# Optimization experiments

Hardware: AMD Instinct MI355X
Metric: run time of the kernel (lower is better)

Reference implementation:

```python
import jax, jax.numpy as jnp
import numpy as np
import math

B, NQ, NK = 8, 1024, 2048
DQ = DK = DV = 1024
H = 8
DH = DV // H
EPS = 1e-5


def _layernorm(x, g, b):
    mu = jnp.mean(x, axis=-1, keepdims=True)
    var = jnp.mean(jnp.square(x - mu), axis=-1, keepdims=True)
    return (x - mu) * jax.lax.rsqrt(var + EPS) * g + b


def setup_inputs() -> dict:
    key = jax.random.key(0)
    ks = jax.random.split(key, 12)
    s_q = 1.0 / math.sqrt(DQ)
    s_v = 1.0 / math.sqrt(DV)
    return {
        "Q": jax.random.normal(ks[0], (B, NQ, DQ), jnp.float32),
        "K": jax.random.normal(ks[1], (B, NK, DK), jnp.float32),
        "Wq": jax.random.normal(ks[2], (DQ, DV), jnp.float32) * s_q,
        "bq": jnp.zeros((DV,), jnp.float32),
        "Wk": jax.random.normal(ks[3], (DK, DV), jnp.float32) * s_q,
        "bk": jnp.zeros((DV,), jnp.float32),
        "Wv": jax.random.normal(ks[4], (DK, DV), jnp.float32) * s_q,
        "bv": jnp.zeros((DV,), jnp.float32),
        "Wo": jax.random.normal(ks[5], (DV, DV), jnp.float32) * s_v,
        "bo": jnp.zeros((DV,), jnp.float32),
        "g0": jnp.ones((DV,), jnp.float32),
        "b0": jnp.zeros((DV,), jnp.float32),
        "g1": jnp.ones((DV,), jnp.float32),
        "b1": jnp.zeros((DV,), jnp.float32),
    }


def reference(Q, K, Wq, bq, Wk, bk, Wv, bv, Wo, bo, g0, b0, g1, b1):
    # projections
    q = Q @ Wq + bq                      # [B, NQ, DV]
    k = K @ Wk + bk                      # [B, NK, DV]
    v = K @ Wv + bv                      # [B, NK, DV]
    qh = q.reshape(B, NQ, H, DH)
    kh = k.reshape(B, NK, H, DH)
    vh = v.reshape(B, NK, H, DH)
    # NOTE: original scales by sqrt(dim_V), not sqrt(d_head)
    scale = 1.0 / math.sqrt(DV)
    logits = jnp.einsum("bqhd,bkhd->bhqk", qh, kh) * scale
    A = jax.nn.softmax(logits, axis=-1)
    # residual baked into attention output: Q_ + A @ V_
    Oh = qh + jnp.einsum("bhqk,bkhd->bqhd", A, vh)
    O = Oh.reshape(B, NQ, DV)
    O = _layernorm(O, g0, b0)
    O = O + jax.nn.relu(O @ Wo + bo)
    O = _layernorm(O, g1, b1)
    return O
```

## Files before the change

kernel.cpp:

```cpp
#include <hip/hip_runtime.h>
#include <stdint.h>

#define DEVI static __device__ __forceinline__

typedef __attribute__((ext_vector_type(8))) short short8;
typedef __attribute__((ext_vector_type(4))) float floatx4;
typedef __attribute__((ext_vector_type(4))) unsigned short ushortx4;

DEVI unsigned short f2bf(float f) {
  union { float f; uint32_t u; } v; v.f = f;
  uint32_t r = v.u + 0x7FFFu + ((v.u >> 16) & 1u);
  return (unsigned short)(r >> 16);
}
DEVI float bf2f(unsigned short s) {
  union { uint32_t u; float f; } v; v.u = ((uint32_t)s) << 16;
  return v.f;
}

DEVI void lds_cp16(void* lds, const void* g) {
  __builtin_amdgcn_global_load_lds(
      (const __attribute__((address_space(1))) uint32_t*)g,
      reinterpret_cast<__attribute__((address_space(3))) uint32_t*>(
          (uint32_t)reinterpret_cast<uintptr_t>(lds)),
      16, 0, 0);
}

__global__ __launch_bounds__(256) void cvt_qk(const float* __restrict__ Q,
                                              const float* __restrict__ K,
                                              unsigned short* __restrict__ Qb,
                                              unsigned short* __restrict__ Kb) {
  const int bid = blockIdx.x;
  const float* src;
  unsigned short* dst;
  size_t i;
  if (bid < 8192) { src = Q; dst = Qb; i = (size_t)bid * 256 + threadIdx.x; }
  else            { src = K; dst = Kb; i = (size_t)(bid - 8192) * 256 + threadIdx.x; }
  const floatx4 v = ((const floatx4*)src)[i];
  ushortx4 o;
  o.x = f2bf(v.x); o.y = f2bf(v.y); o.z = f2bf(v.z); o.w = f2bf(v.w);
  ((ushortx4*)dst)[i] = o;
}

__global__ __launch_bounds__(256) void wtrans4(const float* __restrict__ Wq,
                                               const float* __restrict__ Wk,
                                               const float* __restrict__ Wv,
                                               const float* __restrict__ Wo,
                                               unsigned short* __restrict__ Wt) {
  __shared__ float t[32][33];
  const int tx = threadIdx.x, ty = threadIdx.y;
  const int z = blockIdx.z;
  const float* W = (z == 0) ? Wq : (z == 1) ? Wk : (z == 2) ? Wv : Wo;
  unsigned short* D = Wt + (size_t)z * 1024 * 1024;
  const int c0 = blockIdx.x * 32, r0 = blockIdx.y * 32;
#pragma unroll
  for (int i = 0; i < 4; i++)
    t[ty + i * 8][tx] = W[(size_t)(r0 + ty + i * 8) * 1024 + c0 + tx];
  __syncthreads();
#pragma unroll
  for (int i = 0; i < 4; i++)
    D[(size_t)(c0 + ty + i * 8) * 1024 + r0 + tx] = f2bf(t[tx][ty + i * 8]);
}

template <int EPI>
__global__ __launch_bounds__(256, 3) void gemm_bt(
    const unsigned short* __restrict__ A, const unsigned short* __restrict__ Bt,
    const float* __restrict__ bias, const unsigned short* __restrict__ X1,
    void* __restrict__ Cout) {
  __shared__ unsigned short As[2][4][128][8];
  __shared__ unsigned short Bs[2][4][128][8];

  const int tid = threadIdx.x;
  const int lane = tid & 63, w = tid >> 6;
  const int wr = w >> 1, wc = w & 1;
  const int qd = lane >> 4, l16 = lane & 15;
  const int bid = blockIdx.x;
  const int xcd = bid & 7, loc = bid >> 3;
  const int m0 = (xcd * 8 + (loc & 7)) * 128;
  const int n0 = (loc >> 3) * 128;

  floatx4 acc[4][4];
#pragma unroll
  for (int i = 0; i < 4; i++)
#pragma unroll
    for (int j = 0; j < 4; j++) { floatx4 z = {0.f, 0.f, 0.f, 0.f}; acc[i][j] = z; }

  const int prow = tid & 127;
  const unsigned short* aptr = A + (size_t)(m0 + prow) * 1024 + ((tid >> 7) << 3);
  const unsigned short* bptr = Bt + (size_t)(n0 + prow) * 1024 + ((tid >> 7) << 3);
  const int dstoff = tid * 8;

  lds_cp16(&As[0][0][0][0] + dstoff, aptr);
  lds_cp16(&As[0][0][0][0] + dstoff + 2048, aptr + 16);
  lds_cp16(&Bs[0][0][0][0] + dstoff, bptr);
  lds_cp16(&Bs[0][0][0][0] + dstoff + 2048, bptr + 16);

  for (int it = 0; it < 32; it++) {
    __syncthreads();
    if (it < 31) {
      const int nb = (it + 1) & 1, k0 = (it + 1) * 32;
      lds_cp16(&As[nb][0][0][0] + dstoff, aptr + k0);
      lds_cp16(&As[nb][0][0][0] + dstoff + 2048, aptr + k0 + 16);
      lds_cp16(&Bs[nb][0][0][0] + dstoff, bptr + k0);
      lds_cp16(&Bs[nb][0][0][0] + dstoff + 2048, bptr + k0 + 16);
    }
    const int cur = it & 1;
    short8 af[4], bf[4];
#pragma unroll
    for (int mi = 0; mi < 4; mi++)
      af[mi] = *(const short8*)&As[cur][qd][wr * 64 + mi * 16 + l16][0];
#pragma unroll
    for (int ni = 0; ni < 4; ni++)
      bf[ni] = *(const short8*)&Bs[cur][qd][wc * 64 + ni * 16 + l16][0];
#pragma unroll
    for (int mi = 0; mi < 4; mi++)
#pragma unroll
      for (int ni = 0; ni < 4; ni++)
        acc[mi][ni] =
            __builtin_amdgcn_mfma_f32_16x16x32_bf16(af[mi], bf[ni], acc[mi][ni], 0, 0, 0);
  }

#pragma unroll
  for (int mi = 0; mi < 4; mi++) {
#pragma unroll
    for (int ni = 0; ni < 4; ni++) {
      const int row = m0 + wr * 64 + mi * 16 + qd * 4;
      const int col = n0 + wc * 64 + ni * 16 + l16;
      const float bv = bias[col];
      if constexpr (EPI == 0) {
        unsigned short* C = (unsigned short*)Cout;
#pragma unroll
        for (int r = 0; r < 4; r++)
          C[(size_t)(row + r) * 1024 + col] = f2bf(acc[mi][ni][r] + bv);
      } else {
        float* C = (float*)Cout;
#pragma unroll
        for (int r = 0; r < 4; r++) {
          const float x1 = bf2f(X1[(size_t)(row + r) * 1024 + col]);
          C[(size_t)(row + r) * 1024 + col] = x1 + fmaxf(acc[mi][ni][r] + bv, 0.f);
        }
      }
    }
  }
}

__global__ __launch_bounds__(512, 2) void gemm_kv(
    const unsigned short* __restrict__ A, const unsigned short* __restrict__ Bt,
    const float* __restrict__ biasK, const float* __restrict__ biasV,
    unsigned short* __restrict__ CK, unsigned short* __restrict__ CV) {
  __shared__ unsigned short As[2][4][256][8];
  __shared__ unsigned short Bs[2][4][256][8];

  const int tid = threadIdx.x;
  const int lane = tid & 63, w = tid >> 6;
  const int wr = w & 1, wc = w >> 1;
  const int qd = lane >> 4, l16 = lane & 15;
  const int bid = blockIdx.x;
  const int xcd = bid & 7, loc = bid >> 3;
  const int m0 = (xcd * 8 + (loc & 7)) * 256;
  const int n0 = (loc >> 3) * 256;

  floatx4 acc[8][4];
#pragma unroll
  for (int i = 0; i < 8; i++)
#pragma unroll
    for (int j = 0; j < 4; j++) { floatx4 z = {0.f, 0.f, 0.f, 0.f}; acc[i][j] = z; }

  const int r0 = tid & 255, c0 = tid >> 8;
  const unsigned short* aptr = A + (size_t)(m0 + r0) * 1024 + c0 * 8;
  const unsigned short* bptr = Bt + (size_t)(n0 + r0) * 1024 + c0 * 8;
  unsigned short* dstA = &As[0][c0][r0][0];
  unsigned short* dstB = &Bs[0][c0][r0][0];

  lds_cp16(dstA, aptr);
  lds_cp16(dstA + 4096, aptr + 16);
  lds_cp16(dstB, bptr);
  lds_cp16(dstB + 4096, bptr + 16);

  for (int it = 0; it < 32; it++) {
    __syncthreads();
    if (it < 31) {
      const int nb = (it + 1) & 1, k0 = (it + 1) * 32;
      lds_cp16(dstA + nb * 8192, aptr + k0);
      lds_cp16(dstA + nb * 8192 + 4096, aptr + k0 + 16);
      lds_cp16(dstB + nb * 8192, bptr + k0);
      lds_cp16(dstB + nb * 8192 + 4096, bptr + k0 + 16);
    }
    const int cur = it & 1;
    short8 af[8], bf[4];
#pragma unroll
    for (int mi = 0; mi < 8; mi++)
      af[mi] = *(const short8*)&As[cur][qd][wr * 128 + mi * 16 + l16][0];
#pragma unroll
    for (int ni = 0; ni < 4; ni++)
      bf[ni] = *(const short8*)&Bs[cur][qd][wc * 64 + ni * 16 + l16][0];
#pragma unroll
    for (int mi = 0; mi < 8; mi++)
#pragma unroll
      for (int ni = 0; ni < 4; ni++)
        acc[mi][ni] =
            __builtin_amdgcn_mfma_f32_16x16x32_bf16(af[mi], bf[ni], acc[mi][ni], 0, 0, 0);
  }

#pragma unroll
  for (int mi = 0; mi < 8; mi++) {
#pragma unroll
    for (int ni = 0; ni < 4; ni++) {
      const int row = m0 + wr * 128 + mi * 16 + qd * 4;
      const int col = n0 + wc * 64 + ni * 16 + l16;
      if (col < 1024) {
        const float bv = biasK[col];
#pragma unroll
        for (int r = 0; r < 4; r++)
          CK[(size_t)(row + r) * 1024 + col] = f2bf(acc[mi][ni][r] + bv);
      } else {
        const int vc = col - 1024;
        const float bv = biasV[vc];
        const int bb = row >> 11, nk = row & 2047;
        const int hh = vc >> 7, dh = vc & 127;
        ushortx4 pk;
        pk.x = f2bf(acc[mi][ni][0] + bv);
        pk.y = f2bf(acc[mi][ni][1] + bv);
        pk.z = f2bf(acc[mi][ni][2] + bv);
        pk.w = f2bf(acc[mi][ni][3] + bv);
        *(ushortx4*)&CV[(size_t)((bb * 8 + hh) * 128 + dh) * 2048 + nk] = pk;
      }
    }
  }
}

__global__ __launch_bounds__(256, 2) void attn(
    const unsigned short* __restrict__ qb, const unsigned short* __restrict__ kb,
    const unsigned short* __restrict__ vt, unsigned short* __restrict__ Ob) {
  __shared__ unsigned short smem[32768];

  const int tid = threadIdx.x;
  const int lane = tid & 63, w = tid >> 6;
  const int qd = lane >> 4, l16 = lane & 15;
  const int bid = blockIdx.x;
  const int qt = bid >> 6, bh = bid & 63;
  const int h = bh >> 3, b = bh & 7;
  const int m0 = qt * 128;

  const size_t qbase = ((size_t)(b * 1024 + m0)) * 1024 + h * 128;
  const size_t kbase = ((size_t)(b * 2048)) * 1024 + h * 128;
  const size_t vbase = ((size_t)((b * 8 + h) * 128)) * 2048;

#pragma unroll
  for (int i = 0; i < 8; i++) {
    const int p = i * 256 + tid;
    const int row = p & 127, c = p >> 7;
    lds_cp16(&smem[c * 1024 + row * 8], qb + qbase + (size_t)row * 1024 + c * 8);
  }
#pragma unroll
  for (int i = 0; i < 2; i++) {
    const int p = i * 256 + tid;
    const int kr = p & 31, kc = p >> 5;
    lds_cp16(&smem[16384 + kc * 256 + kr * 8], kb + kbase + (size_t)kr * 1024 + kc * 8);
    const int dh = p & 127, vc = p >> 7;
    lds_cp16(&smem[24576 + vc * 1024 + dh * 8], vt + vbase + (size_t)dh * 2048 + vc * 8);
  }
  __syncthreads();

  short8 qf[2][4];
#pragma unroll
  for (int mi = 0; mi < 2; mi++)
#pragma unroll
    for (int ks = 0; ks < 4; ks++)
      qf[mi][ks] =
          *(const short8*)&smem[(ks * 4 + qd) * 1024 + ((w * 2 + mi) * 16 + l16) * 8];
  __syncthreads();

  floatx4 oacc[2][8];
#pragma unroll
  for (int mi = 0; mi < 2; mi++)
#pragma unroll
    for (int ni = 0; ni < 8; ni++) { floatx4 z = {0.f, 0.f, 0.f, 0.f}; oacc[mi][ni] = z; }
  float lsum[2][4];
#pragma unroll
  for (int mi = 0; mi < 2; mi++)
#pragma unroll
    for (int r = 0; r < 4; r++) lsum[mi][r] = 0.f;

  for (int it = 0; it < 64; it++) {
    if (it) __syncthreads();
    if (it + 1 < 64) {
      const int nb = (it + 1) & 1, kv0 = (it + 1) * 32;
#pragma unroll
      for (int i = 0; i < 2; i++) {
        const int p = i * 256 + tid;
        const int kr = p & 31, kc = p >> 5;
        lds_cp16(&smem[16384 + nb * 4096 + kc * 256 + kr * 8],
                 kb + kbase + (size_t)(kv0 + kr) * 1024 + kc * 8);
        const int dh = p & 127, vc = p >> 7;
        lds_cp16(&smem[24576 + nb * 4096 + vc * 1024 + dh * 8],
                 vt + vbase + (size_t)dh * 2048 + kv0 + vc * 8);
      }
    }
    const int cur = it & 1;

    floatx4 sacc[2][2];
#pragma unroll
    for (int mi = 0; mi < 2; mi++)
#pragma unroll
      for (int ni = 0; ni < 2; ni++) { floatx4 z = {0.f, 0.f, 0.f, 0.f}; sacc[mi][ni] = z; }
#pragma unroll
    for (int ks = 0; ks < 4; ks++) {
      short8 b0 = *(const short8*)&smem[16384 + cur * 4096 + (ks * 4 + qd) * 256 + l16 * 8];
      short8 b1 =
          *(const short8*)&smem[16384 + cur * 4096 + (ks * 4 + qd) * 256 + (16 + l16) * 8];
#pragma unroll
      for (int mi = 0; mi < 2; mi++) {
        sacc[mi][0] = __builtin_amdgcn_mfma_f32_16x16x32_bf16(qf[mi][ks], b0, sacc[mi][0], 0, 0, 0);
        sacc[mi][1] = __builtin_amdgcn_mfma_f32_16x16x32_bf16(qf[mi][ks], b1, sacc[mi][1], 0, 0, 0);
      }
    }

#pragma unroll
    for (int mi = 0; mi < 2; mi++)
#pragma unroll
      for (int ni = 0; ni < 2; ni++) {
        const int kvl = ni * 16 + l16;
#pragma unroll
        for (int r = 0; r < 4; r++) {
          const float e = __expf(sacc[mi][ni][r] * 0.03125f);
          lsum[mi][r] += e;
          smem[(kvl >> 3) * 1024 + ((w * 2 + mi) * 16 + qd * 4 + r) * 8 + (kvl & 7)] = f2bf(e);
        }
      }

    short8 pf[2];
#pragma unroll
    for (int mi = 0; mi < 2; mi++)
      pf[mi] = *(const short8*)&smem[qd * 1024 + ((w * 2 + mi) * 16 + l16) * 8];
#pragma unroll
    for (int ni = 0; ni < 8; ni++) {
      const short8 vf = *(const short8*)&smem[24576 + cur * 4096 + qd * 1024 + (ni * 16 + l16) * 8];
#pragma unroll
      for (int mi = 0; mi < 2; mi++)
        oacc[mi][ni] = __builtin_amdgcn_mfma_f32_16x16x32_bf16(pf[mi], vf, oacc[mi][ni], 0, 0, 0);
    }
  }

  float inv[2][4];
#pragma unroll
  for (int mi = 0; mi < 2; mi++)
#pragma unroll
    for (int r = 0; r < 4; r++) {
      float s = lsum[mi][r];
      s += __shfl_xor(s, 1); s += __shfl_xor(s, 2);
      s += __shfl_xor(s, 4); s += __shfl_xor(s, 8);
      inv[mi][r] = 1.f / s;
    }

#pragma unroll
  for (int mi = 0; mi < 2; mi++)
#pragma unroll
    for (int ni = 0; ni < 8; ni++)
#pragma unroll
      for (int r = 0; r < 4; r++) {
        const int m = (w * 2 + mi) * 16 + qd * 4 + r;
        const int dh = ni * 16 + l16;
        const float qv = bf2f(qb[qbase + (size_t)m * 1024 + dh]);
        Ob[qbase + (size_t)m * 1024 + dh] = f2bf(qv + oacc[mi][ni][r] * inv[mi][r]);
      }
}

__global__ __launch_bounds__(256) void ln_rows(const unsigned short* __restrict__ X,
                                               const float* __restrict__ g,
                                               const float* __restrict__ bb,
                                               unsigned short* __restrict__ Y) {
  __shared__ float red[8];
  const int row = blockIdx.x, tid = threadIdx.x;
  const int w = tid >> 6, lane = tid & 63;
  const ushortx4 u = ((const ushortx4*)(X + (size_t)row * 1024))[tid];
  float x0 = bf2f(u.x), x1 = bf2f(u.y), x2 = bf2f(u.z), x3 = bf2f(u.w);
  float s = x0 + x1 + x2 + x3;
  float s2 = x0 * x0 + x1 * x1 + x2 * x2 + x3 * x3;
#pragma unroll
  for (int off = 1; off < 64; off <<= 1) { s += __shfl_xor(s, off); s2 += __shfl_xor(s2, off); }
  if (lane == 0) { red[w] = s; red[4 + w] = s2; }
  __syncthreads();
  s = red[0] + red[1] + red[2] + red[3];
  s2 = red[4] + red[5] + red[6] + red[7];
  const float mu = s * (1.f / 1024.f);
  const float rs = rsqrtf(s2 * (1.f / 1024.f) - mu * mu + 1e-5f);
  const floatx4 gv = ((const floatx4*)g)[tid];
  const floatx4 bv = ((const floatx4*)bb)[tid];
  ushortx4 o;
  o.x = f2bf((x0 - mu) * rs * gv.x + bv.x);
  o.y = f2bf((x1 - mu) * rs * gv.y + bv.y);
  o.z = f2bf((x2 - mu) * rs * gv.z + bv.z);
  o.w = f2bf((x3 - mu) * rs * gv.w + bv.w);
  ((ushortx4*)(Y + (size_t)row * 1024))[tid] = o;
}

__global__ __launch_bounds__(256) void ln_f32(const float* __restrict__ X,
                                              const float* __restrict__ g,
                                              const float* __restrict__ bb,
                                              float* __restrict__ out) {
  __shared__ float red[8];
  const int row = blockIdx.x, tid = threadIdx.x;
  const int w = tid >> 6, lane = tid & 63;
  const floatx4 xv = ((const floatx4*)(X + (size_t)row * 1024))[tid];
  float x0 = xv.x, x1 = xv.y, x2 = xv.z, x3 = xv.w;
  float s = x0 + x1 + x2 + x3;
  float s2 = x0 * x0 + x1 * x1 + x2 * x2 + x3 * x3;
#pragma unroll
  for (int off = 1; off < 64; off <<= 1) { s += __shfl_xor(s, off); s2 += __shfl_xor(s2, off); }
  if (lane == 0) { red[w] = s; red[4 + w] = s2; }
  __syncthreads();
  s = red[0] + red[1] + red[2] + red[3];
  s2 = red[4] + red[5] + red[6] + red[7];
  const float mu = s * (1.f / 1024.f);
  const float rs = rsqrtf(s2 * (1.f / 1024.f) - mu * mu + 1e-5f);
  const floatx4 gv = ((const floatx4*)g)[tid];
  const floatx4 bv = ((const floatx4*)bb)[tid];
  floatx4 o;
  o.x = (x0 - mu) * rs * gv.x + bv.x;
  o.y = (x1 - mu) * rs * gv.y + bv.y;
  o.z = (x2 - mu) * rs * gv.z + bv.z;
  o.w = (x3 - mu) * rs * gv.w + bv.w;
  ((floatx4*)(out + (size_t)row * 1024))[tid] = o;
}

extern "C" void kernel_launch(void* const* d_in, const int* in_sizes, int n_in,
                              void* d_out, int out_size, void* d_ws, size_t ws_size,
                              hipStream_t stream) {
  (void)in_sizes; (void)n_in; (void)out_size; (void)ws_size;
  const float* Q  = (const float*)d_in[0];
  const float* K  = (const float*)d_in[1];
  const float* Wq = (const float*)d_in[2];
  const float* bq = (const float*)d_in[3];
  const float* Wk = (const float*)d_in[4];
  const float* bk = (const float*)d_in[5];
  const float* Wv = (const float*)d_in[6];
  const float* bv = (const float*)d_in[7];
  const float* Wo = (const float*)d_in[8];
  const float* bo = (const float*)d_in[9];
  const float* g0 = (const float*)d_in[10];
  const float* b0 = (const float*)d_in[11];
  const float* g1 = (const float*)d_in[12];
  const float* b1 = (const float*)d_in[13];
  float* out = (float*)d_out;

  char* ws = (char*)d_ws;
  const size_t MB = 1u << 20;
  unsigned short* Qb  = (unsigned short*)(ws + 0);
  unsigned short* Kb  = (unsigned short*)(ws + 16 * MB);
  unsigned short* Wt  = (unsigned short*)(ws + 48 * MB);
  unsigned short* qbp = (unsigned short*)(ws + 56 * MB);
  unsigned short* kbp = (unsigned short*)(ws + 72 * MB);
  unsigned short* vtp = (unsigned short*)(ws + 104 * MB);
  unsigned short* O   = Qb;
  unsigned short* X1  = Kb;
  float* O2 = (float*)(ws + 72 * MB);

  unsigned short* Wqt  = Wt;
  unsigned short* Wkvt = Wt + (size_t)1024 * 1024;
  unsigned short* Wot  = Wt + (size_t)3072 * 1024;

  cvt_qk<<<24576, 256, 0, stream>>>(Q, K, Qb, Kb);
  wtrans4<<<dim3(32, 32, 4), dim3(32, 8), 0, stream>>>(Wq, Wk, Wv, Wo, Wt);

  gemm_bt<0><<<512, 256, 0, stream>>>(Qb, Wqt, bq, nullptr, qbp);
  gemm_kv<<<512, 512, 0, stream>>>(Kb, Wkvt, bk, bv, kbp, vtp);
  attn<<<512, 256, 0, stream>>>(qbp, kbp, vtp, O);
  ln_rows<<<8192, 256, 0, stream>>>(O, g0, b0, X1);
  gemm_bt<2><<<512, 256, 0, stream>>>(X1, Wot, bo, X1, O2);
  ln_f32<<<8192, 256, 0, stream>>>(O2, g1, b1, out);
}
```

Before: 478.7 us.

## Replace LDS-staged GEMM and attention loads with direct global register loads

Removes the LDS double-buffering (global_load_lds plus syncthreads) from the Q/O projection GEMMs, the KV projection GEMM and the attention kernel. Each wave now loads its MFMA fragments straight from global memory into registers, with a two-stage register ping-pong in the GEMMs. The KV GEMM also moves from 256x256 tiles with 512 threads to 128x128 tiles with 256 threads. This drops barrier and LDS traffic, but loses the cross-wave data sharing that LDS gave, so global and L2 traffic and uncoalesced 16-byte row loads increase.

New measurement: 800.5 us. 1.67x slower.

```diff
diff --git a/kernel.cpp b/kernel.cpp
--- a/kernel.cpp
+++ b/kernel.cpp
@@ -15,14 +15,6 @@
 DEVI float bf2f(unsigned short s) {
   union { uint32_t u; float f; } v; v.u = ((uint32_t)s) << 16;
   return v.f;
-}
-
-DEVI void lds_cp16(void* lds, const void* g) {
-  __builtin_amdgcn_global_load_lds(
-      (const __attribute__((address_space(1))) uint32_t*)g,
-      reinterpret_cast<__attribute__((address_space(3))) uint32_t*>(
-          (uint32_t)reinterpret_cast<uintptr_t>(lds)),
-      16, 0, 0);
 }
 
 __global__ __launch_bounds__(256) void cvt_qk(const float* __restrict__ Q,
@@ -61,22 +53,38 @@
     D[(size_t)(c0 + ty + i * 8) * 1024 + r0 + tx] = f2bf(t[tx][ty + i * 8]);
 }
 
-template <int EPI>
-__global__ __launch_bounds__(256, 3) void gemm_bt(
+#define LD_AB(av, bv, K0)                                                      \
+  {                                                                            \
+    _Pragma("unroll") for (int i = 0; i < 4; i++) {                            \
+      av[i] = *(const short8*)(ap + (size_t)i * 16384 + (K0));                 \
+      bv[i] = *(const short8*)(bp + (size_t)i * 16384 + (K0));                 \
+    }                                                                          \
+  }
+#define MFMA16(av, bv)                                                         \
+  {                                                                            \
+    _Pragma("unroll") for (int mi = 0; mi < 4; mi++)                           \
+        _Pragma("unroll") for (int ni = 0; ni < 4; ni++) acc[mi][ni] =         \
+        __builtin_amdgcn_mfma_f32_16x16x32_bf16(av[mi], bv[ni], acc[mi][ni],   \
+                                                0, 0, 0);                      \
+  }
+
+template <int EPI, int BSH>
+__global__ __launch_bounds__(256, 2) void gemm_rd(
     const unsigned short* __restrict__ A, const unsigned short* __restrict__ Bt,
     const float* __restrict__ bias, const unsigned short* __restrict__ X1,
     void* __restrict__ Cout) {
-  __shared__ unsigned short As[2][4][128][8];
-  __shared__ unsigned short Bs[2][4][128][8];
-
   const int tid = threadIdx.x;
   const int lane = tid & 63, w = tid >> 6;
   const int wr = w >> 1, wc = w & 1;
   const int qd = lane >> 4, l16 = lane & 15;
   const int bid = blockIdx.x;
   const int xcd = bid & 7, loc = bid >> 3;
-  const int m0 = (xcd * 8 + (loc & 7)) * 128;
-  const int n0 = (loc >> 3) * 128;
+  const int mt = xcd * (1 << BSH) + (loc & ((1 << BSH) - 1));
+  const int nt = loc >> BSH;
+  const int m0 = mt * 128, n0 = nt * 128;
+
+  const unsigned short* ap = A + (size_t)(m0 + wr * 64 + l16) * 1024 + qd * 8;
+  const unsigned short* bp = Bt + (size_t)(n0 + wc * 64 + l16) * 1024 + qd * 8;
 
   floatx4 acc[4][4];
 #pragma unroll
@@ -84,39 +92,13 @@
 #pragma unroll
     for (int j = 0; j < 4; j++) { floatx4 z = {0.f, 0.f, 0.f, 0.f}; acc[i][j] = z; }
 
-  const int prow = tid & 127;
-  const unsigned short* aptr = A + (size_t)(m0 + prow) * 1024 + ((tid >> 7) << 3);
-  const unsigned short* bptr = Bt + (size_t)(n0 + prow) * 1024 + ((tid >> 7) << 3);
-  const int dstoff = tid * 8;
-
-  lds_cp16(&As[0][0][0][0] + dstoff, aptr);
-  lds_cp16(&As[0][0][0][0] + dstoff + 2048, aptr + 16);
-  lds_cp16(&Bs[0][0][0][0] + dstoff, bptr);
-  lds_cp16(&Bs[0][0][0][0] + dstoff + 2048, bptr + 16);
-
-  for (int it = 0; it < 32; it++) {
-    __syncthreads();
-    if (it < 31) {
-      const int nb = (it + 1) & 1, k0 = (it + 1) * 32;
-      lds_cp16(&As[nb][0][0][0] + dstoff, aptr + k0);
-      lds_cp16(&As[nb][0][0][0] + dstoff + 2048, aptr + k0 + 16);
-      lds_cp16(&Bs[nb][0][0][0] + dstoff, bptr + k0);
-      lds_cp16(&Bs[nb][0][0][0] + dstoff + 2048, bptr + k0 + 16);
-    }
-    const int cur = it & 1;
-    short8 af[4], bf[4];
-#pragma unroll
-    for (int mi = 0; mi < 4; mi++)
-      af[mi] = *(const short8*)&As[cur][qd][wr * 64 + mi * 16 + l16][0];
-#pragma unroll
-    for (int ni = 0; ni < 4; ni++)
-      bf[ni] = *(const short8*)&Bs[cur][qd][wc * 64 + ni * 16 + l16][0];
-#pragma unroll
-    for (int mi = 0; mi < 4; mi++)
-#pragma unroll
-      for (int ni = 0; ni < 4; ni++)
-        acc[mi][ni] =
-            __builtin_amdgcn_mfma_f32_16x16x32_bf16(af[mi], bf[ni], acc[mi][ni], 0, 0, 0);
+  short8 a0[4], b0[4], a1[4], b1[4];
+  LD_AB(a0, b0, 0)
+  for (int it = 0; it < 32; it += 2) {
+    LD_AB(a1, b1, (it + 1) * 32)
+    MFMA16(a0, b0)
+    if (it + 2 < 32) LD_AB(a0, b0, (it + 2) * 32)
+    MFMA16(a1, b1)
   }
 
 #pragma unroll
@@ -143,69 +125,43 @@
   }
 }
 
-__global__ __launch_bounds__(512, 2) void gemm_kv(
+__global__ __launch_bounds__(256, 2) void gemm_kv_rd(
     const unsigned short* __restrict__ A, const unsigned short* __restrict__ Bt,
     const float* __restrict__ biasK, const float* __restrict__ biasV,
     unsigned short* __restrict__ CK, unsigned short* __restrict__ CV) {
-  __shared__ unsigned short As[2][4][256][8];
-  __shared__ unsigned short Bs[2][4][256][8];
-
   const int tid = threadIdx.x;
   const int lane = tid & 63, w = tid >> 6;
-  const int wr = w & 1, wc = w >> 1;
+  const int wr = w >> 1, wc = w & 1;
   const int qd = lane >> 4, l16 = lane & 15;
   const int bid = blockIdx.x;
   const int xcd = bid & 7, loc = bid >> 3;
-  const int m0 = (xcd * 8 + (loc & 7)) * 256;
-  const int n0 = (loc >> 3) * 256;
-
-  floatx4 acc[8][4];
-#pragma unroll
-  for (int i = 0; i < 8; i++)
+  const int mt = xcd * 16 + (loc & 15);
+  const int nt = loc >> 4;
+  const int m0 = mt * 128, n0 = nt * 128;
+
+  const unsigned short* ap = A + (size_t)(m0 + wr * 64 + l16) * 1024 + qd * 8;
+  const unsigned short* bp = Bt + (size_t)(n0 + wc * 64 + l16) * 1024 + qd * 8;
+
+  floatx4 acc[4][4];
+#pragma unroll
+  for (int i = 0; i < 4; i++)
 #pragma unroll
     for (int j = 0; j < 4; j++) { floatx4 z = {0.f, 0.f, 0.f, 0.f}; acc[i][j] = z; }
 
-  const int r0 = tid & 255, c0 = tid >> 8;
-  const unsigned short* aptr = A + (size_t)(m0 + r0) * 1024 + c0 * 8;
-  const unsigned short* bptr = Bt + (size_t)(n0 + r0) * 1024 + c0 * 8;
-  unsigned short* dstA = &As[0][c0][r0][0];
-  unsigned short* dstB = &Bs[0][c0][r0][0];
-
-  lds_cp16(dstA, aptr);
-  lds_cp16(dstA + 4096, aptr + 16);
-  lds_cp16(dstB, bptr);
-  lds_cp16(dstB + 4096, bptr + 16);
-
-  for (int it = 0; it < 32; it++) {
-    __syncthreads();
-    if (it < 31) {
-      const int nb = (it + 1) & 1, k0 = (it + 1) * 32;
-      lds_cp16(dstA + nb * 8192, aptr + k0);
-      lds_cp16(dstA + nb * 8192 + 4096, aptr + k0 + 16);
-      lds_cp16(dstB + nb * 8192, bptr + k0);
-      lds_cp16(dstB + nb * 8192 + 4096, bptr + k0 + 16);
-    }
-    const int cur = it & 1;
-    short8 af[8], bf[4];
-#pragma unroll
-    for (int mi = 0; mi < 8; mi++)
-      af[mi] = *(const short8*)&As[cur][qd][wr * 128 + mi * 16 + l16][0];
-#pragma unroll
-    for (int ni = 0; ni < 4; ni++)
-      bf[ni] = *(const short8*)&Bs[cur][qd][wc * 64 + ni * 16 + l16][0];
-#pragma unroll
-    for (int mi = 0; mi < 8; mi++)
-#pragma unroll
-      for (int ni = 0; ni < 4; ni++)
-        acc[mi][ni] =
-            __builtin_amdgcn_mfma_f32_16x16x32_bf16(af[mi], bf[ni], acc[mi][ni], 0, 0, 0);
-  }
-
-#pragma unroll
-  for (int mi = 0; mi < 8; mi++) {
+  short8 a0[4], b0[4], a1[4], b1[4];
+  LD_AB(a0, b0, 0)
+  for (int it = 0; it < 32; it += 2) {
+    LD_AB(a1, b1, (it + 1) * 32)
+    MFMA16(a0, b0)
+    if (it + 2 < 32) LD_AB(a0, b0, (it + 2) * 32)
+    MFMA16(a1, b1)
+  }
+
+#pragma unroll
+  for (int mi = 0; mi < 4; mi++) {
 #pragma unroll
     for (int ni = 0; ni < 4; ni++) {
-      const int row = m0 + wr * 128 + mi * 16 + qd * 4;
+      const int row = m0 + wr * 64 + mi * 16 + qd * 4;
       const int col = n0 + wc * 64 + ni * 16 + l16;
       if (col < 1024) {
         const float bv = biasK[col];
@@ -231,7 +187,7 @@
 __global__ __launch_bounds__(256, 2) void attn(
     const unsigned short* __restrict__ qb, const unsigned short* __restrict__ kb,
     const unsigned short* __restrict__ vt, unsigned short* __restrict__ Ob) {
-  __shared__ unsigned short smem[32768];
+  __shared__ unsigned short Ps[4096];
 
   const int tid = threadIdx.x;
   const int lane = tid & 63, w = tid >> 6;
@@ -245,30 +201,16 @@
   const size_t kbase = ((size_t)(b * 2048)) * 1024 + h * 128;
   const size_t vbase = ((size_t)((b * 8 + h) * 128)) * 2048;
 
-#pragma unroll
-  for (int i = 0; i < 8; i++) {
-    const int p = i * 256 + tid;
-    const int row = p & 127, c = p >> 7;
-    lds_cp16(&smem[c * 1024 + row * 8], qb + qbase + (size_t)row * 1024 + c * 8);
-  }
-#pragma unroll
-  for (int i = 0; i < 2; i++) {
-    const int p = i * 256 + tid;
-    const int kr = p & 31, kc = p >> 5;
-    lds_cp16(&smem[16384 + kc * 256 + kr * 8], kb + kbase + (size_t)kr * 1024 + kc * 8);
-    const int dh = p & 127, vc = p >> 7;
-    lds_cp16(&smem[24576 + vc * 1024 + dh * 8], vt + vbase + (size_t)dh * 2048 + vc * 8);
-  }
-  __syncthreads();
-
+  const unsigned short* qp = qb + qbase + (size_t)(w * 32 + l16) * 1024 + qd * 8;
   short8 qf[2][4];
 #pragma unroll
   for (int mi = 0; mi < 2; mi++)
 #pragma unroll
     for (int ks = 0; ks < 4; ks++)
-      qf[mi][ks] =
-          *(const short8*)&smem[(ks * 4 + qd) * 1024 + ((w * 2 + mi) * 16 + l16) * 8];
-  __syncthreads();
+      qf[mi][ks] = *(const short8*)(qp + (size_t)mi * 16384 + ks * 32);
+
+  const unsigned short* kp = kb + kbase + (size_t)l16 * 1024 + qd * 8;
+  const unsigned short* vp = vt + vbase + (size_t)l16 * 2048 + qd * 8;
 
   floatx4 oacc[2][8];
 #pragma unroll
@@ -282,21 +224,7 @@
     for (int r = 0; r < 4; r++) lsum[mi][r] = 0.f;
 
   for (int it = 0; it < 64; it++) {
-    if (it) __syncthreads();
-    if (it + 1 < 64) {
-      const int nb = (it + 1) & 1, kv0 = (it + 1) * 32;
-#pragma unroll
-      for (int i = 0; i < 2; i++) {
-        const int p = i * 256 + tid;
-        const int kr = p & 31, kc = p >> 5;
-        lds_cp16(&smem[16384 + nb * 4096 + kc * 256 + kr * 8],
-                 kb + kbase + (size_t)(kv0 + kr) * 1024 + kc * 8);
-        const int dh = p & 127, vc = p >> 7;
-        lds_cp16(&smem[24576 + nb * 4096 + vc * 1024 + dh * 8],
-                 vt + vbase + (size_t)dh * 2048 + kv0 + vc * 8);
-      }
-    }
-    const int cur = it & 1;
+    const int kv0 = it * 32;
 
     floatx4 sacc[2][2];
 #pragma unroll
@@ -305,13 +233,12 @@
       for (int ni = 0; ni < 2; ni++) { floatx4 z = {0.f, 0.f, 0.f, 0.f}; sacc[mi][ni] = z; }
 #pragma unroll
     for (int ks = 0; ks < 4; ks++) {
-      short8 b0 = *(const short8*)&smem[16384 + cur * 4096 + (ks * 4 + qd) * 256 + l16 * 8];
-      short8 b1 =
-          *(const short8*)&smem[16384 + cur * 4096 + (ks * 4 + qd) * 256 + (16 + l16) * 8];
+      const short8 k0f = *(const short8*)(kp + (size_t)kv0 * 1024 + ks * 32);
+      const short8 k1f = *(const short8*)(kp + (size_t)(kv0 + 16) * 1024 + ks * 32);
 #pragma unroll
       for (int mi = 0; mi < 2; mi++) {
-        sacc[mi][0] = __builtin_amdgcn_mfma_f32_16x16x32_bf16(qf[mi][ks], b0, sacc[mi][0], 0, 0, 0);
-        sacc[mi][1] = __builtin_amdgcn_mfma_f32_16x16x32_bf16(qf[mi][ks], b1, sacc[mi][1], 0, 0, 0);
+        sacc[mi][0] = __builtin_amdgcn_mfma_f32_16x16x32_bf16(qf[mi][ks], k0f, sacc[mi][0], 0, 0, 0);
+        sacc[mi][1] = __builtin_amdgcn_mfma_f32_16x16x32_bf16(qf[mi][ks], k1f, sacc[mi][1], 0, 0, 0);
       }
     }
 
@@ -324,17 +251,17 @@
         for (int r = 0; r < 4; r++) {
           const float e = __expf(sacc[mi][ni][r] * 0.03125f);
           lsum[mi][r] += e;
-          smem[(kvl >> 3) * 1024 + ((w * 2 + mi) * 16 + qd * 4 + r) * 8 + (kvl & 7)] = f2bf(e);
+          Ps[(kvl >> 3) * 1024 + (w * 32 + mi * 16 + qd * 4 + r) * 8 + (kvl & 7)] = f2bf(e);
         }
       }
 
     short8 pf[2];
 #pragma unroll
     for (int mi = 0; mi < 2; mi++)
-      pf[mi] = *(const short8*)&smem[qd * 1024 + ((w * 2 + mi) * 16 + l16) * 8];
+      pf[mi] = *(const short8*)&Ps[qd * 1024 + (w * 32 + mi * 16 + l16) * 8];
 #pragma unroll
     for (int ni = 0; ni < 8; ni++) {
-      const short8 vf = *(const short8*)&smem[24576 + cur * 4096 + qd * 1024 + (ni * 16 + l16) * 8];
+      const short8 vf = *(const short8*)(vp + (size_t)ni * 32768 + kv0);
 #pragma unroll
       for (int mi = 0; mi < 2; mi++)
         oacc[mi][ni] = __builtin_amdgcn_mfma_f32_16x16x32_bf16(pf[mi], vf, oacc[mi][ni], 0, 0, 0);
@@ -358,7 +285,7 @@
     for (int ni = 0; ni < 8; ni++)
 #pragma unroll
       for (int r = 0; r < 4; r++) {
-        const int m = (w * 2 + mi) * 16 + qd * 4 + r;
+        const int m = w * 32 + mi * 16 + qd * 4 + r;
         const int dh = ni * 16 + l16;
         const float qv = bf2f(qb[qbase + (size_t)m * 1024 + dh]);
         Ob[qbase + (size_t)m * 1024 + dh] = f2bf(qv + oacc[mi][ni][r] * inv[mi][r]);
@@ -462,10 +389,10 @@
   cvt_qk<<<24576, 256, 0, stream>>>(Q, K, Qb, Kb);
   wtrans4<<<dim3(32, 32, 4), dim3(32, 8), 0, stream>>>(Wq, Wk, Wv, Wo, Wt);
 
-  gemm_bt<0><<<512, 256, 0, stream>>>(Qb, Wqt, bq, nullptr, qbp);
-  gemm_kv<<<512, 512, 0, stream>>>(Kb, Wkvt, bk, bv, kbp, vtp);
+  gemm_rd<0, 3><<<512, 256, 0, stream>>>(Qb, Wqt, bq, nullptr, qbp);
+  gemm_kv_rd<<<2048, 256, 0, stream>>>(Kb, Wkvt, bk, bv, kbp, vtp);
   attn<<<512, 256, 0, stream>>>(qbp, kbp, vtp, O);
   ln_rows<<<8192, 256, 0, stream>>>(O, g0, b0, X1);
-  gemm_bt<2><<<512, 256, 0, stream>>>(X1, Wot, bo, X1, O2);
+  gemm_rd<2, 3><<<512, 256, 0, stream>>>(X1, Wot, bo, X1, O2);
   ln_f32<<<8192, 256, 0, stream>>>(O2, g1, b1, out);
 }
```

## Run K/V projection GEMM in FP8 with smaller tiles

Applied to the files above, without the earlier changes.

Converts K and the Wk/Wv weights to FP8 instead of bf16 and replaces the bf16 K/V projection GEMM with an FP8 MFMA kernel using 128x128 tiles, 256 threads and 2048 blocks. This halves the bytes for the K input and weights and doubles MFMA throughput per instruction. The workspace layout is rearranged accordingly. It risks accuracy loss from FP8 quantisation of K and the weights, which feed both the attention logits and the values.

New measurement: 437.9 us. -8.5%, faster.

```diff
diff --git a/kernel.cpp b/kernel.cpp
--- a/kernel.cpp
+++ b/kernel.cpp
@@ -15,6 +15,9 @@
 DEVI float bf2f(unsigned short s) {
   union { uint32_t u; float f; } v; v.u = ((uint32_t)s) << 16;
   return v.f;
+}
+DEVI unsigned char f2fp8(float f) {
+  return (unsigned char)(__builtin_amdgcn_cvt_pk_fp8_f32(f, f, 0, false) & 0xff);
 }
 
 DEVI void lds_cp16(void* lds, const void* g) {
@@ -28,37 +31,49 @@
 __global__ __launch_bounds__(256) void cvt_qk(const float* __restrict__ Q,
                                               const float* __restrict__ K,
                                               unsigned short* __restrict__ Qb,
-                                              unsigned short* __restrict__ Kb) {
+                                              unsigned char* __restrict__ Kf8) {
   const int bid = blockIdx.x;
-  const float* src;
-  unsigned short* dst;
-  size_t i;
-  if (bid < 8192) { src = Q; dst = Qb; i = (size_t)bid * 256 + threadIdx.x; }
-  else            { src = K; dst = Kb; i = (size_t)(bid - 8192) * 256 + threadIdx.x; }
-  const floatx4 v = ((const floatx4*)src)[i];
-  ushortx4 o;
-  o.x = f2bf(v.x); o.y = f2bf(v.y); o.z = f2bf(v.z); o.w = f2bf(v.w);
-  ((ushortx4*)dst)[i] = o;
+  if (bid < 8192) {
+    const size_t i = (size_t)bid * 256 + threadIdx.x;
+    const floatx4 v = ((const floatx4*)Q)[i];
+    ushortx4 o;
+    o.x = f2bf(v.x); o.y = f2bf(v.y); o.z = f2bf(v.z); o.w = f2bf(v.w);
+    ((ushortx4*)Qb)[i] = o;
+  } else {
+    const size_t i = (size_t)(bid - 8192) * 256 + threadIdx.x;
+    const floatx4 v = ((const floatx4*)K)[i];
+    int p = __builtin_amdgcn_cvt_pk_fp8_f32(v.x, v.y, 0, false);
+    p = __builtin_amdgcn_cvt_pk_fp8_f32(v.z, v.w, p, true);
+    ((int*)Kf8)[i] = p;
+  }
 }
 
 __global__ __launch_bounds__(256) void wtrans4(const float* __restrict__ Wq,
                                                const float* __restrict__ Wk,
                                                const float* __restrict__ Wv,
                                                const float* __restrict__ Wo,
-                                               unsigned short* __restrict__ Wt) {
+                                               unsigned short* __restrict__ Wt,
+                                               unsigned char* __restrict__ Wt8) {
   __shared__ float t[32][33];
   const int tx = threadIdx.x, ty = threadIdx.y;
   const int z = blockIdx.z;
   const float* W = (z == 0) ? Wq : (z == 1) ? Wk : (z == 2) ? Wv : Wo;
-  unsigned short* D = Wt + (size_t)z * 1024 * 1024;
   const int c0 = blockIdx.x * 32, r0 = blockIdx.y * 32;
 #pragma unroll
   for (int i = 0; i < 4; i++)
     t[ty + i * 8][tx] = W[(size_t)(r0 + ty + i * 8) * 1024 + c0 + tx];
   __syncthreads();
-#pragma unroll
-  for (int i = 0; i < 4; i++)
-    D[(size_t)(c0 + ty + i * 8) * 1024 + r0 + tx] = f2bf(t[tx][ty + i * 8]);
+  if (z == 0 || z == 3) {
+    unsigned short* D = Wt + (z == 0 ? 0 : (size_t)1024 * 1024);
+#pragma unroll
+    for (int i = 0; i < 4; i++)
+      D[(size_t)(c0 + ty + i * 8) * 1024 + r0 + tx] = f2bf(t[tx][ty + i * 8]);
+  } else {
+    unsigned char* D = Wt8 + (z == 1 ? 0 : (size_t)1024 * 1024);
+#pragma unroll
+    for (int i = 0; i < 4; i++)
+      D[(size_t)(c0 + ty + i * 8) * 1024 + r0 + tx] = f2fp8(t[tx][ty + i * 8]);
+  }
 }
 
 template <int EPI>
@@ -143,69 +158,82 @@
   }
 }
 
-__global__ __launch_bounds__(512, 2) void gemm_kv(
-    const unsigned short* __restrict__ A, const unsigned short* __restrict__ Bt,
+__global__ __launch_bounds__(256, 3) void gemm_kv_f8(
+    const unsigned char* __restrict__ A, const unsigned char* __restrict__ Bt,
     const float* __restrict__ biasK, const float* __restrict__ biasV,
     unsigned short* __restrict__ CK, unsigned short* __restrict__ CV) {
-  __shared__ unsigned short As[2][4][256][8];
-  __shared__ unsigned short Bs[2][4][256][8];
+  __shared__ unsigned char As[2][4][128][16];
+  __shared__ unsigned char Bs[2][4][128][16];
 
   const int tid = threadIdx.x;
   const int lane = tid & 63, w = tid >> 6;
-  const int wr = w & 1, wc = w >> 1;
+  const int wr = w >> 1, wc = w & 1;
   const int qd = lane >> 4, l16 = lane & 15;
   const int bid = blockIdx.x;
   const int xcd = bid & 7, loc = bid >> 3;
-  const int m0 = (xcd * 8 + (loc & 7)) * 256;
-  const int n0 = (loc >> 3) * 256;
-
-  floatx4 acc[8][4];
-#pragma unroll
-  for (int i = 0; i < 8; i++)
+  const int m0 = (xcd * 16 + (loc & 15)) * 128;
+  const int n0 = (loc >> 4) * 128;
+
+  floatx4 acc[4][4];
+#pragma unroll
+  for (int i = 0; i < 4; i++)
 #pragma unroll
     for (int j = 0; j < 4; j++) { floatx4 z = {0.f, 0.f, 0.f, 0.f}; acc[i][j] = z; }
 
-  const int r0 = tid & 255, c0 = tid >> 8;
-  const unsigned short* aptr = A + (size_t)(m0 + r0) * 1024 + c0 * 8;
-  const unsigned short* bptr = Bt + (size_t)(n0 + r0) * 1024 + c0 * 8;
-  unsigned short* dstA = &As[0][c0][r0][0];
-  unsigned short* dstB = &Bs[0][c0][r0][0];
-
-  lds_cp16(dstA, aptr);
-  lds_cp16(dstA + 4096, aptr + 16);
-  lds_cp16(dstB, bptr);
-  lds_cp16(dstB + 4096, bptr + 16);
-
-  for (int it = 0; it < 32; it++) {
+  const int srow = tid & 127, sc = tid >> 7;
+  const unsigned char* aptr = A + (size_t)(m0 + srow) * 1024 + sc * 16;
+  const unsigned char* bptr = Bt + (size_t)(n0 + srow) * 1024 + sc * 16;
+  unsigned char* dA = &As[0][sc][srow][0];
+  unsigned char* dB = &Bs[0][sc][srow][0];
+
+  lds_cp16(dA, aptr);
+  lds_cp16(dA + 4096, aptr + 32);
+  lds_cp16(dB, bptr);
+  lds_cp16(dB + 4096, bptr + 32);
+
+  for (int it = 0; it < 16; it++) {
     __syncthreads();
-    if (it < 31) {
-      const int nb = (it + 1) & 1, k0 = (it + 1) * 32;
-      lds_cp16(dstA + nb * 8192, aptr + k0);
-      lds_cp16(dstA + nb * 8192 + 4096, aptr + k0 + 16);
-      lds_cp16(dstB + nb * 8192, bptr + k0);
-      lds_cp16(dstB + nb * 8192 + 4096, bptr + k0 + 16);
+    if (it < 15) {
+      const int nb = (it + 1) & 1, k0 = (it + 1) * 64;
+      lds_cp16(dA + nb * 8192, aptr + k0);
+      lds_cp16(dA + nb * 8192 + 4096, aptr + k0 + 32);
+      lds_cp16(dB + nb * 8192, bptr + k0);
+      lds_cp16(dB + nb * 8192 + 4096, bptr + k0 + 32);
     }
     const int cur = it & 1;
-    short8 af[8], bf[4];
-#pragma unroll
-    for (int mi = 0; mi < 8; mi++)
-      af[mi] = *(const short8*)&As[cur][qd][wr * 128 + mi * 16 + l16][0];
-#pragma unroll
-    for (int ni = 0; ni < 4; ni++)
-      bf[ni] = *(const short8*)&Bs[cur][qd][wc * 64 + ni * 16 + l16][0];
-#pragma unroll
-    for (int mi = 0; mi < 8; mi++)
+    const int coff = (qd & 1) * 8, chi = qd >> 1;
+    long a8[4][2], b8[4][2];
+#pragma unroll
+    for (int mi = 0; mi < 4; mi++) {
+      const int row = wr * 64 + mi * 16 + l16;
+      a8[mi][0] = *(const long*)&As[cur][chi][row][coff];
+      a8[mi][1] = *(const long*)&As[cur][2 + chi][row][coff];
+    }
+#pragma unroll
+    for (int ni = 0; ni < 4; ni++) {
+      const int row = wc * 64 + ni * 16 + l16;
+      b8[ni][0] = *(const long*)&Bs[cur][chi][row][coff];
+      b8[ni][1] = *(const long*)&Bs[cur][2 + chi][row][coff];
+    }
+#pragma unroll
+    for (int mi = 0; mi < 4; mi++)
 #pragma unroll
       for (int ni = 0; ni < 4; ni++)
-        acc[mi][ni] =
-            __builtin_amdgcn_mfma_f32_16x16x32_bf16(af[mi], bf[ni], acc[mi][ni], 0, 0, 0);
-  }
-
-#pragma unroll
-  for (int mi = 0; mi < 8; mi++) {
+        acc[mi][ni] = __builtin_amdgcn_mfma_f32_16x16x32_fp8_fp8(
+            a8[mi][0], b8[ni][0], acc[mi][ni], 0, 0, 0);
+#pragma unroll
+    for (int mi = 0; mi < 4; mi++)
+#pragma unroll
+      for (int ni = 0; ni < 4; ni++)
+        acc[mi][ni] = __builtin_amdgcn_mfma_f32_16x16x32_fp8_fp8(
+            a8[mi][1], b8[ni][1], acc[mi][ni], 0, 0, 0);
+  }
+
+#pragma unroll
+  for (int mi = 0; mi < 4; mi++) {
 #pragma unroll
     for (int ni = 0; ni < 4; ni++) {
-      const int row = m0 + wr * 128 + mi * 16 + qd * 4;
+      const int row = m0 + wr * 64 + mi * 16 + qd * 4;
       const int col = n0 + wc * 64 + ni * 16 + l16;
       if (col < 1024) {
         const float bv = biasK[col];
@@ -446,24 +474,24 @@
   char* ws = (char*)d_ws;
   const size_t MB = 1u << 20;
   unsigned short* Qb  = (unsigned short*)(ws + 0);
-  unsigned short* Kb  = (unsigned short*)(ws + 16 * MB);
-  unsigned short* Wt  = (unsigned short*)(ws + 48 * MB);
-  unsigned short* qbp = (unsigned short*)(ws + 56 * MB);
-  unsigned short* kbp = (unsigned short*)(ws + 72 * MB);
-  unsigned short* vtp = (unsigned short*)(ws + 104 * MB);
+  unsigned short* X1  = (unsigned short*)(ws + 16 * MB);
+  unsigned short* Wt  = (unsigned short*)(ws + 32 * MB);
+  unsigned char*  Wt8 = (unsigned char*)(ws + 36 * MB);
+  unsigned char*  Kf8 = (unsigned char*)(ws + 38 * MB);
+  unsigned short* qbp = (unsigned short*)(ws + 54 * MB);
+  unsigned short* kbp = (unsigned short*)(ws + 70 * MB);
+  unsigned short* vtp = (unsigned short*)(ws + 102 * MB);
   unsigned short* O   = Qb;
-  unsigned short* X1  = Kb;
-  float* O2 = (float*)(ws + 72 * MB);
-
-  unsigned short* Wqt  = Wt;
-  unsigned short* Wkvt = Wt + (size_t)1024 * 1024;
-  unsigned short* Wot  = Wt + (size_t)3072 * 1024;
-
-  cvt_qk<<<24576, 256, 0, stream>>>(Q, K, Qb, Kb);
-  wtrans4<<<dim3(32, 32, 4), dim3(32, 8), 0, stream>>>(Wq, Wk, Wv, Wo, Wt);
+  float* O2 = (float*)(ws + 70 * MB);
+
+  unsigned short* Wqt = Wt;
+  unsigned short* Wot = Wt + (size_t)1024 * 1024;
+
+  cvt_qk<<<24576, 256, 0, stream>>>(Q, K, Qb, Kf8);
+  wtrans4<<<dim3(32, 32, 4), dim3(32, 8), 0, stream>>>(Wq, Wk, Wv, Wo, Wt, Wt8);
 
   gemm_bt<0><<<512, 256, 0, stream>>>(Qb, Wqt, bq, nullptr, qbp);
-  gemm_kv<<<512, 512, 0, stream>>>(Kb, Wkvt, bk, bv, kbp, vtp);
+  gemm_kv_f8<<<2048, 256, 0, stream>>>(Kf8, Wt8, bk, bv, kbp, vtp);
   attn<<<512, 256, 0, stream>>>(qbp, kbp, vtp, O);
   ln_rows<<<8192, 256, 0, stream>>>(O, g0, b0, X1);
   gemm_bt<2><<<512, 256, 0, stream>>>(X1, Wot, bo, X1, O2);
```
